# Optimization experiments

Measured on AMD Instinct MI355X. Metric: run time of the kernel, lower is better.

## Reference

```python
import jax, jax.numpy as jnp
import numpy as np

B, N, E, H, D, FF, L = 64, 200, 128, 8, 16, 512, 6
S = N + 1  # depot + nodes
EPS = 1e-5


def setup_inputs() -> dict:
    key = jax.random.key(0)
    ks = jax.random.split(key, 24)
    r = jax.random.normal
    HD = H * D
    inp = {
        "depot_xy": jax.random.uniform(ks[0], (B, 1, 3), dtype=jnp.float32),
        "node_xy_demand_tw": jax.random.uniform(ks[1], (B, N, 4), dtype=jnp.float32),
        "route_attn": r(ks[2], (B, H, S, S), dtype=jnp.float32),
        # initial embeddings
        "Wd": r(ks[3], (3, E)) * 0.3, "bd": jnp.zeros((E,)),
        "Wn": r(ks[4], (4, E)) * 0.3, "bn": jnp.zeros((E,)),
        # per-layer stacked params (leading dim L)
        "Wq": r(ks[5], (L, E, HD)) / np.sqrt(E),
        "Wk": r(ks[6], (L, E, HD)) / np.sqrt(E),
        "Wv": r(ks[7], (L, E, HD)) / np.sqrt(E),
        "Wo": r(ks[8], (L, HD, E)) / np.sqrt(HD), "bo": jnp.zeros((L, E)),
        # score_aggr MLP: in=head_num*aspect_num=2H, hidden=2H, out=H
        "A1w": r(ks[9], (L, 2 * H, 2 * H)) / np.sqrt(2 * H), "A1b": jnp.zeros((L, 2 * H)),
        "A2w": r(ks[10], (L, 2 * H, H)) / np.sqrt(2 * H), "A2b": jnp.zeros((L, H)),
        # instance-norm affine params
        "n1w": jnp.ones((L, E)), "n1b": jnp.zeros((L, E)),
        "n2w": jnp.ones((L, E)), "n2b": jnp.zeros((L, E)),
        # feed-forward
        "F1w": r(ks[11], (L, E, FF)) / np.sqrt(E), "F1b": jnp.zeros((L, FF)),
        "F2w": r(ks[12], (L, FF, E)) / np.sqrt(FF), "F2b": jnp.zeros((L, E)),
    }
    return inp


def _inorm(y, w, b):
    # InstanceNorm1d over the sequence axis (per batch, per channel), biased var, eps=1e-5
    m = jnp.mean(y, axis=1, keepdims=True)
    v = jnp.var(y, axis=1, keepdims=True)
    return (y - m) / jnp.sqrt(v + EPS) * w + b


def _encoder(depot_xy, node_xy_demand_tw, route_attn, Wd, bd, Wn, bn,
             Wq, Wk, Wv, Wo, bo, A1w, A1b, A2w, A2b,
             n1w, n1b, n2w, n2b, F1w, F1b, F2w, F2b):
    x = jnp.concatenate([depot_xy @ Wd + bd, node_xy_demand_tw @ Wn + bn], axis=1)  # [B,S,E]
    b, s = x.shape[0], x.shape[1]
    for l in range(L):
        heads = lambda t: t.reshape(b, s, H, D).transpose(0, 2, 1, 3)  # [B,H,S,D]
        q, k, v = heads(x @ Wq[l]), heads(x @ Wk[l]), heads(x @ Wv[l])
        score = jnp.einsum('bhnd,bhmd->bhnm', q, k)                    # [B,H,S,S]
        cat = jnp.concatenate([score, route_attn], axis=1)             # [B,2H,S,S]
        cat = cat.transpose(0, 2, 3, 1)                                # [B,S,S,2H]
        agg = jax.nn.relu(cat @ A1w[l] + A1b[l]) @ A2w[l] + A2b[l]     # [B,S,S,H]
        scaled = agg.transpose(0, 3, 1, 2)                             # [B,H,S,S]
        w = jax.nn.softmax(scaled, axis=-1)
        o = jnp.einsum('bhnm,bhmd->bhnd', w, v)                        # [B,H,S,D]
        o = o.transpose(0, 2, 1, 3).reshape(b, s, H * D)
        mh = o @ Wo[l] + bo[l]
        out1 = _inorm(x + mh, n1w[l], n1b[l])
        ff = jax.nn.relu(out1 @ F1w[l] + F1b[l]) @ F2w[l] + F2b[l]
        x = _inorm(out1 + ff, n2w[l], n2b[l])
    return x


def reference(depot_xy, node_xy_demand_tw, route_attn, Wd, bd, Wn, bn,
              Wq, Wk, Wv, Wo, bo, A1w, A1b, A2w, A2b,
              n1w, n1b, n2w, n2b, F1w, F1b, F2w, F2b):
    return _encoder(depot_xy, node_xy_demand_tw, route_attn, Wd, bd, Wn, bn,
                    Wq, Wk, Wv, Wo, bo, A1w, A1b, A2w, A2b,
                    n1w, n1b, n2w, n2b, F1w, F1b, F2w, F2b)
```

## Files before the change

kernel.cpp:

```cpp
#include <hip/hip_runtime.h>
#include <hip/hip_bf16.h>

#define B_   64
#define N_   200
#define S_   201
#define E_   128
#define H_   8
#define D_   16
#define HD_  128
#define FF_  512
#define L_   6
#define TWOH_ 16
#define NCH_  4
#define NCHB_ 51
#define PADM_ 209

typedef __hip_bfloat16 bf16;
typedef __attribute__((ext_vector_type(8))) short bfrag;
typedef __attribute__((ext_vector_type(4))) float f32x4;

__device__ __forceinline__ void split_bf16(float v, bf16& h, bf16& l) {
  h = __float2bfloat16(v);
  l = __float2bfloat16(v - __bfloat162float(h));
}

__global__ void embed_kernel(const float* __restrict__ depot, const float* __restrict__ node,
                             const float* __restrict__ Wd, const float* __restrict__ bd,
                             const float* __restrict__ Wn, const float* __restrict__ bn,
                             float* __restrict__ X, bf16* __restrict__ XBh, bf16* __restrict__ XBl) {
  int idx = blockIdx.x * blockDim.x + threadIdx.x;
  if (idx >= B_ * S_ * E_) return;
  int e  = idx & (E_ - 1);
  int bs = idx >> 7;
  int s  = bs % S_;
  int b  = bs / S_;
  float acc;
  if (s == 0) {
    acc = bd[e];
    #pragma unroll
    for (int i = 0; i < 3; ++i) acc += depot[b * 3 + i] * Wd[i * E_ + e];
  } else {
    acc = bn[e];
    const float* nd = node + ((size_t)b * N_ + (s - 1)) * 4;
    #pragma unroll
    for (int i = 0; i < 4; ++i) acc += nd[i] * Wn[i * E_ + e];
  }
  X[idx] = acc;
  bf16 hh, ll;
  split_bf16(acc, hh, ll);
  XBh[idx] = hh;
  XBl[idx] = ll;
}

__global__ void wcvt_kernel(const float* __restrict__ Wo, const float* __restrict__ F1w,
                            const float* __restrict__ F2w, const float* __restrict__ Wq,
                            const float* __restrict__ Wk, const float* __restrict__ Wv,
                            bf16* __restrict__ WTh, bf16* __restrict__ WTl) {
  int idx = blockIdx.x * blockDim.x + threadIdx.x;
  if (idx >= 1179648) return;
  float v;
  if (idx < 98304) {
    int l = idx / 16384, rr = idx % 16384;
    int e = rr / 128, h = rr % 128;
    v = Wo[(size_t)l * 16384 + h * 128 + e];
  } else if (idx < 491520) {
    int rem = idx - 98304;
    int l = rem / 65536, rr = rem % 65536;
    int f = rr / 128, e = rr % 128;
    v = F1w[(size_t)l * 65536 + e * 512 + f];
  } else if (idx < 884736) {
    int rem = idx - 491520;
    int l = rem / 65536, rr = rem % 65536;
    int e = rr / 512, f = rr % 512;
    v = F2w[(size_t)l * 65536 + f * 128 + e];
  } else if (idx < 1081344) {
    int rem = idx - 884736;
    int l = rem / 32768, rr = rem % 32768;
    int n = rr / 128, e = rr % 128;
    const float* src = (n < 128) ? Wq : Wk;
    int hd = n & 127;
    v = src[(size_t)l * 16384 + e * 128 + hd];
  } else {
    int rem = idx - 1081344;
    int l = rem / 16384, rr = rem % 16384;
    int hd = rr / 128, e = rr % 128;
    v = Wv[(size_t)l * 16384 + e * 128 + hd];
  }
  bf16 h, l2;
  split_bf16(v, h, l2);
  WTh[idx] = h;
  WTl[idx] = l2;
}

template<int EPI>
__global__ __launch_bounds__(256) void mgemm_kernel(
    const bf16* __restrict__ Ah, const bf16* __restrict__ Al,
    const bf16* __restrict__ BTh, const bf16* __restrict__ BTl,
    const float* __restrict__ bias, const float* __restrict__ res,
    float* __restrict__ Cf, bf16* __restrict__ Cbh, bf16* __restrict__ Cbl,
    int K, int Ntot) {
  __shared__ __align__(16) bf16 Ash[64][72];
  __shared__ __align__(16) bf16 Asl[64][72];
  __shared__ __align__(16) bf16 Bsh[64][72];
  __shared__ __align__(16) bf16 Bsl[64][72];
  int tid = threadIdx.x;
  int m0 = blockIdx.x * 64, n0 = blockIdx.y * 64;
  int lane = tid & 63, wave = tid >> 6;
  int wr = wave >> 1, wc = wave & 1;
  int la = lane & 15, lb = lane >> 4;
  f32x4 acc[2][2] = {};
  for (int k0 = 0; k0 < K; k0 += 64) {
    #pragma unroll
    for (int p = 0; p < 2; ++p) {
      int ch = tid + p * 256;
      int r = ch >> 3, kc = (ch & 7) << 3;
      size_t ga = (size_t)(m0 + r) * K + k0 + kc;
      size_t gb = (size_t)(n0 + r) * K + k0 + kc;
      *reinterpret_cast<bfrag*>(&Ash[r][kc]) = *reinterpret_cast<const bfrag*>(&Ah[ga]);
      *reinterpret_cast<bfrag*>(&Asl[r][kc]) = *reinterpret_cast<const bfrag*>(&Al[ga]);
      *reinterpret_cast<bfrag*>(&Bsh[r][kc]) = *reinterpret_cast<const bfrag*>(&BTh[gb]);
      *reinterpret_cast<bfrag*>(&Bsl[r][kc]) = *reinterpret_cast<const bfrag*>(&BTl[gb]);
    }
    __syncthreads();
    #pragma unroll
    for (int ks = 0; ks < 64; ks += 32) {
      bfrag ah0 = *(const bfrag*)&Ash[wr * 32 + la][ks + lb * 8];
      bfrag ah1 = *(const bfrag*)&Ash[wr * 32 + 16 + la][ks + lb * 8];
      bfrag al0 = *(const bfrag*)&Asl[wr * 32 + la][ks + lb * 8];
      bfrag al1 = *(const bfrag*)&Asl[wr * 32 + 16 + la][ks + lb * 8];
      bfrag bh0 = *(const bfrag*)&Bsh[wc * 32 + la][ks + lb * 8];
      bfrag bh1 = *(const bfrag*)&Bsh[wc * 32 + 16 + la][ks + lb * 8];
      bfrag bl0 = *(const bfrag*)&Bsl[wc * 32 + la][ks + lb * 8];
      bfrag bl1 = *(const bfrag*)&Bsl[wc * 32 + 16 + la][ks + lb * 8];
      acc[0][0] = __builtin_amdgcn_mfma_f32_16x16x32_bf16(ah0, bh0, acc[0][0], 0, 0, 0);
      acc[0][0] = __builtin_amdgcn_mfma_f32_16x16x32_bf16(ah0, bl0, acc[0][0], 0, 0, 0);
      acc[0][0] = __builtin_amdgcn_mfma_f32_16x16x32_bf16(al0, bh0, acc[0][0], 0, 0, 0);
      acc[0][1] = __builtin_amdgcn_mfma_f32_16x16x32_bf16(ah0, bh1, acc[0][1], 0, 0, 0);
      acc[0][1] = __builtin_amdgcn_mfma_f32_16x16x32_bf16(ah0, bl1, acc[0][1], 0, 0, 0);
      acc[0][1] = __builtin_amdgcn_mfma_f32_16x16x32_bf16(al0, bh1, acc[0][1], 0, 0, 0);
      acc[1][0] = __builtin_amdgcn_mfma_f32_16x16x32_bf16(ah1, bh0, acc[1][0], 0, 0, 0);
      acc[1][0] = __builtin_amdgcn_mfma_f32_16x16x32_bf16(ah1, bl0, acc[1][0], 0, 0, 0);
      acc[1][0] = __builtin_amdgcn_mfma_f32_16x16x32_bf16(al1, bh0, acc[1][0], 0, 0, 0);
      acc[1][1] = __builtin_amdgcn_mfma_f32_16x16x32_bf16(ah1, bh1, acc[1][1], 0, 0, 0);
      acc[1][1] = __builtin_amdgcn_mfma_f32_16x16x32_bf16(ah1, bl1, acc[1][1], 0, 0, 0);
      acc[1][1] = __builtin_amdgcn_mfma_f32_16x16x32_bf16(al1, bh1, acc[1][1], 0, 0, 0);
    }
    __syncthreads();
  }
  int r0 = lb * 4;
  #pragma unroll
  for (int ti = 0; ti < 2; ++ti)
    #pragma unroll
    for (int tj = 0; tj < 2; ++tj)
      #pragma unroll
      for (int j = 0; j < 4; ++j) {
        int m = m0 + wr * 32 + ti * 16 + r0 + j;
        int n = n0 + wc * 32 + tj * 16 + la;
        float v = acc[ti][tj][j];
        if (EPI == 1) {
          v += bias[n] + res[(size_t)m * Ntot + n];
          Cf[(size_t)m * Ntot + n] = v;
        } else if (EPI == 2) {
          v += bias[n];
          v = v > 0.f ? v : 0.f;
          bf16 vh, vl;
          split_bf16(v, vh, vl);
          Cbh[(size_t)m * Ntot + n] = vh;
          Cbl[(size_t)m * Ntot + n] = vl;
        } else {
          Cf[(size_t)m * Ntot + n] = v;
        }
      }
}

__global__ __launch_bounds__(256) void score_kernel(const float* __restrict__ QK,
                                                    float* __restrict__ SC) {
  int bh = blockIdx.x;
  int h = bh & 7, b = bh >> 3;
  int nbase = blockIdx.y * 51;
  int ncnt = min(51, S_ - nbase);
  __shared__ __align__(16) float qs[51][20];
  __shared__ __align__(16) float ks[S_][20];
  int tid = threadIdx.x;
  for (int p = tid; p < 51 * 16; p += 256) {
    int r = p >> 4, d = p & 15;
    if (r < ncnt) qs[r][d] = QK[((size_t)(b * S_ + nbase + r)) * 256 + h * D_ + d];
  }
  for (int p = tid; p < S_ * 16; p += 256) {
    int r = p >> 4, d = p & 15;
    ks[r][d] = QK[((size_t)(b * S_ + r)) * 256 + 128 + h * D_ + d];
  }
  __syncthreads();
  float* out = SC + ((size_t)(b * H_ + h)) * S_ * S_;
  int tn = tid >> 4, tm = tid & 15;
  for (int n0 = tn * 2; n0 < ncnt; n0 += 32) {
    int n1v = (n0 + 1 < ncnt);
    f32x4 q0[4], q1[4];
    #pragma unroll
    for (int qd = 0; qd < 4; ++qd) {
      q0[qd] = *(const f32x4*)&qs[n0][qd * 4];
      q1[qd] = *(const f32x4*)&qs[n1v ? n0 + 1 : n0][qd * 4];
    }
    for (int m0 = tm * 2; m0 < S_; m0 += 32) {
      int m1v = (m0 + 1 < S_);
      float a00 = 0, a01 = 0, a10 = 0, a11 = 0;
      #pragma unroll
      for (int qd = 0; qd < 4; ++qd) {
        f32x4 k0 = *(const f32x4*)&ks[m0][qd * 4];
        f32x4 k1 = *(const f32x4*)&ks[m1v ? m0 + 1 : m0][qd * 4];
        #pragma unroll
        for (int c = 0; c < 4; ++c) {
          a00 += q0[qd][c] * k0[c];
          a01 += q0[qd][c] * k1[c];
          a10 += q1[qd][c] * k0[c];
          a11 += q1[qd][c] * k1[c];
        }
      }
      int gn = nbase + n0;
      out[(size_t)gn * S_ + m0] = a00;
      if (m1v) out[(size_t)gn * S_ + m0 + 1] = a01;
      if (n1v) {
        out[(size_t)(gn + 1) * S_ + m0] = a10;
        if (m1v) out[(size_t)(gn + 1) * S_ + m0 + 1] = a11;
      }
    }
  }
}

__global__ __launch_bounds__(256) void attn_kernel(
    const float* __restrict__ SC, const float* __restrict__ RA,
    const float* __restrict__ A1w, const float* __restrict__ A1b,
    const float* __restrict__ A2w, const float* __restrict__ A2b,
    const float* __restrict__ V, bf16* __restrict__ OBh, bf16* __restrict__ OBl) {
  int blk = blockIdx.x;
  int b  = blk / NCHB_;
  int n0 = (blk % NCHB_) * NCH_;
  int NV = min(NCH_, S_ - n0);
  __shared__ float PL[NCH_][H_][PADM_];
  __shared__ float partial[2][NCH_][H_][D_];
  __shared__ float inv[NCH_][H_];
  int tid = threadIdx.x;

  {
    float cc[4][TWOH_];
    int   mm[4], nnv[4];
    bool  val[4];
    #pragma unroll
    for (int s = 0; s < 4; ++s) {
      int e = tid + s * 256;
      val[s] = (e < NV * S_);
      int nn = e / S_;
      int m  = e - nn * S_;
      if (!val[s]) { nn = 0; m = 0; }
      nnv[s] = nn; mm[s] = m;
      const float* scp = SC + (((size_t)b * H_) * S_ + (n0 + nn)) * S_ + m;
      const float* rap = RA + (((size_t)b * H_) * S_ + (n0 + nn)) * S_ + m;
      #pragma unroll
      for (int h = 0; h < H_; ++h) {
        cc[s][h]      = scp[(size_t)h * S_ * S_];
        cc[s][H_ + h] = rap[(size_t)h * S_ * S_];
      }
    }
    #pragma unroll
    for (int s = 0; s < 4; ++s) {
      if (!val[s]) continue;
      float h1[TWOH_];
      #pragma unroll
      for (int j = 0; j < TWOH_; ++j) h1[j] = A1b[j];
      #pragma unroll
      for (int i = 0; i < TWOH_; ++i) {
        float c = cc[s][i];
        #pragma unroll
        for (int j = 0; j < TWOH_; ++j)
          h1[j] += c * A1w[i * TWOH_ + j];
      }
      float agg[H_];
      #pragma unroll
      for (int h = 0; h < H_; ++h) agg[h] = A2b[h];
      #pragma unroll
      for (int j = 0; j < TWOH_; ++j) {
        float r = fmaxf(h1[j], 0.f);
        #pragma unroll
        for (int h = 0; h < H_; ++h)
          agg[h] += r * A2w[j * H_ + h];
      }
      #pragma unroll
      for (int h = 0; h < H_; ++h) PL[nnv[s]][h][mm[s]] = agg[h];
    }
  }
  __syncthreads();

  {
    int g = tid >> 3, lane = tid & 7;
    int nn = g >> 3, h = g & 7;
    if (nn < NV) {
      float mx = -1e30f;
      for (int m = lane; m < S_; m += 8) mx = fmaxf(mx, PL[nn][h][m]);
      #pragma unroll
      for (int off = 4; off > 0; off >>= 1) mx = fmaxf(mx, __shfl_xor(mx, off, 8));
      float sum = 0.f;
      for (int m = lane; m < S_; m += 8) {
        float e = __expf(PL[nn][h][m] - mx);
        PL[nn][h][m] = e;
        sum += e;
      }
      #pragma unroll
      for (int off = 4; off > 0; off >>= 1) sum += __shfl_xor(sum, off, 8);
      if (lane == 0) inv[nn][h] = 1.f / sum;
    }
  }
  __syncthreads();

  {
    int half = tid >> 7, h = (tid >> 4) & 7, d = tid & 15;
    float a0 = 0.f, a1 = 0.f, a2 = 0.f, a3 = 0.f;
    const float* vp = V + (size_t)b * S_ * HD_ + h * D_ + d;
    for (int m = half; m < S_; m += 2) {
      float vv = vp[(size_t)m * HD_];
      a0 += PL[0][h][m] * vv;
      a1 += PL[1][h][m] * vv;
      a2 += PL[2][h][m] * vv;
      a3 += PL[3][h][m] * vv;
    }
    partial[half][0][h][d] = a0;
    partial[half][1][h][d] = a1;
    partial[half][2][h][d] = a2;
    partial[half][3][h][d] = a3;
  }
  __syncthreads();
  if (tid < 128) {
    int h = tid >> 4, d = tid & 15;
    #pragma unroll
    for (int nn = 0; nn < NCH_; ++nn)
      if (nn < NV) {
        float s = (partial[0][nn][h][d] + partial[1][nn][h][d]) * inv[nn][h];
        size_t o = ((size_t)b * S_ + (n0 + nn)) * HD_ + h * D_ + d;
        bf16 sh, sl;
        split_bf16(s, sh, sl);
        OBh[o] = sh;
        OBl[o] = sl;
      }
  }
}

__global__ __launch_bounds__(512) void inorm_kernel(const float* __restrict__ Y,
                                                    const float* __restrict__ w,
                                                    const float* __restrict__ bb,
                                                    float* __restrict__ X,
                                                    bf16* __restrict__ XBh,
                                                    bf16* __restrict__ XBl) {
  int b = blockIdx.x;
  int tid = threadIdx.x;
  int e = tid & 127, sg = tid >> 7;
  __shared__ float ps[4][128], pss[4][128];
  const float* base = Y + (size_t)b * S_ * E_;
  float s = 0.f, ss = 0.f;
  for (int i = sg; i < S_; i += 4) {
    float v = base[(size_t)i * E_ + e];
    s += v; ss += v * v;
  }
  ps[sg][e] = s; pss[sg][e] = ss;
  __syncthreads();
  if (sg == 0) {
    s  = ps[0][e] + ps[1][e] + ps[2][e] + ps[3][e];
    ss = pss[0][e] + pss[1][e] + pss[2][e] + pss[3][e];
    float mean = s / S_;
    float var  = fmaxf(ss / S_ - mean * mean, 0.f);
    float scale = rsqrtf(var + 1e-5f) * w[e];
    ps[0][e]  = scale;
    pss[0][e] = bb[e] - mean * scale;
  }
  __syncthreads();
  float scale = ps[0][e], shift = pss[0][e];
  float* dst = X + (size_t)b * S_ * E_;
  for (int i = sg; i < S_; i += 4) {
    size_t idx = (size_t)i * E_ + e;
    float v = base[idx] * scale + shift;
    dst[idx] = v;
    if (XBh) {
      size_t gi = (size_t)b * S_ * E_ + idx;
      bf16 vh, vl;
      split_bf16(v, vh, vl);
      XBh[gi] = vh;
      XBl[gi] = vl;
    }
  }
}

extern "C" void kernel_launch(void* const* d_in, const int* in_sizes, int n_in,
                              void* d_out, int out_size, void* d_ws, size_t ws_size,
                              hipStream_t stream) {
  const float* depot = (const float*)d_in[0];
  const float* node  = (const float*)d_in[1];
  const float* RA    = (const float*)d_in[2];
  const float* Wd    = (const float*)d_in[3];
  const float* bd    = (const float*)d_in[4];
  const float* Wn    = (const float*)d_in[5];
  const float* bn    = (const float*)d_in[6];
  const float* Wq    = (const float*)d_in[7];
  const float* Wk    = (const float*)d_in[8];
  const float* Wv    = (const float*)d_in[9];
  const float* Wo    = (const float*)d_in[10];
  const float* bo    = (const float*)d_in[11];
  const float* A1w   = (const float*)d_in[12];
  const float* A1b   = (const float*)d_in[13];
  const float* A2w   = (const float*)d_in[14];
  const float* A2b   = (const float*)d_in[15];
  const float* n1w   = (const float*)d_in[16];
  const float* n1b   = (const float*)d_in[17];
  const float* n2w   = (const float*)d_in[18];
  const float* n2b   = (const float*)d_in[19];
  const float* F1w   = (const float*)d_in[20];
  const float* F1b   = (const float*)d_in[21];
  const float* F2w   = (const float*)d_in[22];
  const float* F2b   = (const float*)d_in[23];

  const size_t XSZ  = (size_t)B_ * S_ * E_;
  const size_t SCSZ = (size_t)B_ * H_ * S_ * S_;
  const size_t XBF  = XSZ / 2;
  float* ws = (float*)d_ws;
  float* X   = ws;
  float* QK  = ws + XSZ;
  float* V   = ws + 3 * XSZ;
  float* SC  = ws + 4 * XSZ;
  float* TMP = SC;
  bf16*  XBh = (bf16*)(SC + XSZ);
  bf16*  XBl = (bf16*)(SC + XSZ + XBF);
  bf16*  HBh = (bf16*)(SC + XSZ + 2 * XBF);
  bf16*  HBl = (bf16*)(SC + XSZ + 6 * XBF);
  float* tail = ws + 4 * XSZ + SCSZ;
  bf16*  WTh = (bf16*)tail;
  bf16*  WTl = (bf16*)(tail + 589824);
  bf16* OBh = (bf16*)QK;
  bf16* OBl = (bf16*)(ws + 2 * XSZ);

  const int M = B_ * S_;

  wcvt_kernel<<<4608, 256, 0, stream>>>(Wo, F1w, F2w, Wq, Wk, Wv, WTh, WTl);
  embed_kernel<<<(B_ * S_ * E_ + 255) / 256, 256, 0, stream>>>(depot, node, Wd, bd, Wn, bn, X, XBh, XBl);

  for (int l = 0; l < L_; ++l) {
    mgemm_kernel<3><<<dim3(M / 64, 4), 256, 0, stream>>>(
        XBh, XBl, WTh + 884736 + (size_t)l * 32768, WTl + 884736 + (size_t)l * 32768,
        nullptr, nullptr, QK, nullptr, nullptr, E_, 256);
    mgemm_kernel<3><<<dim3(M / 64, 2), 256, 0, stream>>>(
        XBh, XBl, WTh + 1081344 + (size_t)l * 16384, WTl + 1081344 + (size_t)l * 16384,
        nullptr, nullptr, V, nullptr, nullptr, E_, HD_);
    score_kernel<<<dim3(B_ * H_, 4), 256, 0, stream>>>(QK, SC);
    attn_kernel<<<B_ * NCHB_, 256, 0, stream>>>(SC, RA,
        A1w + (size_t)l * TWOH_ * TWOH_, A1b + (size_t)l * TWOH_,
        A2w + (size_t)l * TWOH_ * H_,    A2b + (size_t)l * H_, V, OBh, OBl);
    mgemm_kernel<1><<<dim3(M / 64, 2), 256, 0, stream>>>(
        OBh, OBl, WTh + (size_t)l * 16384, WTl + (size_t)l * 16384,
        bo + (size_t)l * E_, X, TMP, nullptr, nullptr, HD_, E_);
    inorm_kernel<<<B_, 512, 0, stream>>>(TMP, n1w + (size_t)l * E_, n1b + (size_t)l * E_, X, XBh, XBl);
    mgemm_kernel<2><<<dim3(M / 64, 8), 256, 0, stream>>>(
        XBh, XBl, WTh + 98304 + (size_t)l * 65536, WTl + 98304 + (size_t)l * 65536,
        F1b + (size_t)l * FF_, nullptr, nullptr, HBh, HBl, E_, FF_);
    mgemm_kernel<1><<<dim3(M / 64, 2), 256, 0, stream>>>(
        HBh, HBl, WTh + 491520 + (size_t)l * 65536, WTl + 491520 + (size_t)l * 65536,
        F2b + (size_t)l * E_, X, TMP, nullptr, nullptr, FF_, E_);
    float* dst = (l == L_ - 1) ? (float*)d_out : X;
    bf16* xh = (l == L_ - 1) ? nullptr : XBh;
    bf16* xl = (l == L_ - 1) ? nullptr : XBl;
    inorm_kernel<<<B_, 512, 0, stream>>>(TMP, n2w + (size_t)l * E_, n2b + (size_t)l * E_, dst, xh, xl);
  }
}
```

Measured before the change: 1.507 ms.

## Stage attention score rows in shared memory and split instance norm across channels

The attention kernel now handles 2 query rows per block instead of 4, doubling the block count. It first copies the score and route rows into shared memory with coalesced row-contiguous loads, then computes the per-element MLP from shared memory, replacing the strided per-head global gathers. The instance-norm kernel is split across 4 channel blocks per batch with 128 threads each, raising parallelism from 64 blocks to 256. The trade-offs are extra shared memory per block and less reuse of V loads in the attention kernel.

New measurement: 2.673 ms. +77.3%, slower.

```diff
diff --git a/kernel.cpp b/kernel.cpp
--- a/kernel.cpp
+++ b/kernel.cpp
@@ -11,9 +11,10 @@
 #define FF_  512
 #define L_   6
 #define TWOH_ 16
-#define NCH_  4
-#define NCHB_ 51
+#define NCH_  2
+#define NCHB_ 101
 #define PADM_ 209
+#define CATP_ 204
 
 typedef __hip_bfloat16 bf16;
 typedef __attribute__((ext_vector_type(8))) short bfrag;
@@ -236,76 +237,73 @@
   int b  = blk / NCHB_;
   int n0 = (blk % NCHB_) * NCH_;
   int NV = min(NCH_, S_ - n0);
+  __shared__ float cat[NCH_][TWOH_][CATP_];
   __shared__ float PL[NCH_][H_][PADM_];
   __shared__ float partial[2][NCH_][H_][D_];
   __shared__ float inv[NCH_][H_];
   int tid = threadIdx.x;
 
   {
-    float cc[4][TWOH_];
-    int   mm[4], nnv[4];
-    bool  val[4];
-    #pragma unroll
-    for (int s = 0; s < 4; ++s) {
-      int e = tid + s * 256;
-      val[s] = (e < NV * S_);
-      int nn = e / S_;
-      int m  = e - nn * S_;
-      if (!val[s]) { nn = 0; m = 0; }
-      nnv[s] = nn; mm[s] = m;
-      const float* scp = SC + (((size_t)b * H_) * S_ + (n0 + nn)) * S_ + m;
-      const float* rap = RA + (((size_t)b * H_) * S_ + (n0 + nn)) * S_ + m;
-      #pragma unroll
-      for (int h = 0; h < H_; ++h) {
-        cc[s][h]      = scp[(size_t)h * S_ * S_];
-        cc[s][H_ + h] = rap[(size_t)h * S_ * S_];
-      }
-    }
-    #pragma unroll
-    for (int s = 0; s < 4; ++s) {
-      if (!val[s]) continue;
-      float h1[TWOH_];
-      #pragma unroll
-      for (int j = 0; j < TWOH_; ++j) h1[j] = A1b[j];
-      #pragma unroll
-      for (int i = 0; i < TWOH_; ++i) {
-        float c = cc[s][i];
-        #pragma unroll
-        for (int j = 0; j < TWOH_; ++j)
-          h1[j] += c * A1w[i * TWOH_ + j];
-      }
-      float agg[H_];
-      #pragma unroll
-      for (int h = 0; h < H_; ++h) agg[h] = A2b[h];
-      #pragma unroll
-      for (int j = 0; j < TWOH_; ++j) {
-        float r = fmaxf(h1[j], 0.f);
-        #pragma unroll
-        for (int h = 0; h < H_; ++h)
-          agg[h] += r * A2w[j * H_ + h];
-      }
-      #pragma unroll
-      for (int h = 0; h < H_; ++h) PL[nnv[s]][h][mm[s]] = agg[h];
-    }
+    int total = NV * TWOH_ * S_;
+    for (int p = tid; p < total; p += 256) {
+      int r = p / S_;
+      int m = p - r * S_;
+      int nn = r >> 4, i = r & 15;
+      const float* src = (i < H_)
+        ? SC + (((size_t)b * H_ + i) * S_ + (n0 + nn)) * S_
+        : RA + (((size_t)b * H_ + (i - H_)) * S_ + (n0 + nn)) * S_;
+      cat[nn][i][m] = src[m];
+    }
+  }
+  __syncthreads();
+
+  for (int e = tid; e < NV * S_; e += 256) {
+    int nn = (e >= S_) ? 1 : 0;
+    int m  = e - nn * S_;
+    float cc[TWOH_];
+    #pragma unroll
+    for (int i = 0; i < TWOH_; ++i) cc[i] = cat[nn][i][m];
+    float h1[TWOH_];
+    #pragma unroll
+    for (int j = 0; j < TWOH_; ++j) h1[j] = A1b[j];
+    #pragma unroll
+    for (int i = 0; i < TWOH_; ++i) {
+      float c = cc[i];
+      #pragma unroll
+      for (int j = 0; j < TWOH_; ++j)
+        h1[j] += c * A1w[i * TWOH_ + j];
+    }
+    float agg[H_];
+    #pragma unroll
+    for (int h = 0; h < H_; ++h) agg[h] = A2b[h];
+    #pragma unroll
+    for (int j = 0; j < TWOH_; ++j) {
+      float r = fmaxf(h1[j], 0.f);
+      #pragma unroll
+      for (int h = 0; h < H_; ++h)
+        agg[h] += r * A2w[j * H_ + h];
+    }
+    #pragma unroll
+    for (int h = 0; h < H_; ++h) PL[nn][h][m] = agg[h];
   }
   __syncthreads();
 
   {
-    int g = tid >> 3, lane = tid & 7;
+    int g = tid >> 4, lane = tid & 15;
     int nn = g >> 3, h = g & 7;
     if (nn < NV) {
       float mx = -1e30f;
-      for (int m = lane; m < S_; m += 8) mx = fmaxf(mx, PL[nn][h][m]);
-      #pragma unroll
-      for (int off = 4; off > 0; off >>= 1) mx = fmaxf(mx, __shfl_xor(mx, off, 8));
+      for (int m = lane; m < S_; m += 16) mx = fmaxf(mx, PL[nn][h][m]);
+      #pragma unroll
+      for (int off = 8; off > 0; off >>= 1) mx = fmaxf(mx, __shfl_xor(mx, off, 16));
       float sum = 0.f;
-      for (int m = lane; m < S_; m += 8) {
+      for (int m = lane; m < S_; m += 16) {
         float e = __expf(PL[nn][h][m] - mx);
         PL[nn][h][m] = e;
         sum += e;
       }
       #pragma unroll
-      for (int off = 4; off > 0; off >>= 1) sum += __shfl_xor(sum, off, 8);
+      for (int off = 8; off > 0; off >>= 1) sum += __shfl_xor(sum, off, 16);
       if (lane == 0) inv[nn][h] = 1.f / sum;
     }
   }
@@ -313,19 +311,15 @@
 
   {
     int half = tid >> 7, h = (tid >> 4) & 7, d = tid & 15;
-    float a0 = 0.f, a1 = 0.f, a2 = 0.f, a3 = 0.f;
+    float a0 = 0.f, a1 = 0.f;
     const float* vp = V + (size_t)b * S_ * HD_ + h * D_ + d;
     for (int m = half; m < S_; m += 2) {
       float vv = vp[(size_t)m * HD_];
       a0 += PL[0][h][m] * vv;
       a1 += PL[1][h][m] * vv;
-      a2 += PL[2][h][m] * vv;
-      a3 += PL[3][h][m] * vv;
     }
     partial[half][0][h][d] = a0;
     partial[half][1][h][d] = a1;
-    partial[half][2][h][d] = a2;
-    partial[half][3][h][d] = a3;
   }
   __syncthreads();
   if (tid < 128) {
@@ -343,35 +337,37 @@
   }
 }
 
-__global__ __launch_bounds__(512) void inorm_kernel(const float* __restrict__ Y,
+__global__ __launch_bounds__(128) void inorm_kernel(const float* __restrict__ Y,
                                                     const float* __restrict__ w,
                                                     const float* __restrict__ bb,
                                                     float* __restrict__ X,
                                                     bf16* __restrict__ XBh,
                                                     bf16* __restrict__ XBl) {
   int b = blockIdx.x;
+  int e0 = blockIdx.y * 32;
   int tid = threadIdx.x;
-  int e = tid & 127, sg = tid >> 7;
-  __shared__ float ps[4][128], pss[4][128];
+  int el = tid & 31, sg = tid >> 5;
+  int e = e0 + el;
+  __shared__ float ps[4][32], pss[4][32];
   const float* base = Y + (size_t)b * S_ * E_;
   float s = 0.f, ss = 0.f;
   for (int i = sg; i < S_; i += 4) {
     float v = base[(size_t)i * E_ + e];
     s += v; ss += v * v;
   }
-  ps[sg][e] = s; pss[sg][e] = ss;
+  ps[sg][el] = s; pss[sg][el] = ss;
   __syncthreads();
   if (sg == 0) {
-    s  = ps[0][e] + ps[1][e] + ps[2][e] + ps[3][e];
-    ss = pss[0][e] + pss[1][e] + pss[2][e] + pss[3][e];
+    s  = ps[0][el] + ps[1][el] + ps[2][el] + ps[3][el];
+    ss = pss[0][el] + pss[1][el] + pss[2][el] + pss[3][el];
     float mean = s / S_;
     float var  = fmaxf(ss / S_ - mean * mean, 0.f);
     float scale = rsqrtf(var + 1e-5f) * w[e];
-    ps[0][e]  = scale;
-    pss[0][e] = bb[e] - mean * scale;
-  }
-  __syncthreads();
-  float scale = ps[0][e], shift = pss[0][e];
+    ps[0][el]  = scale;
+    pss[0][el] = bb[e] - mean * scale;
+  }
+  __syncthreads();
+  float scale = ps[0][el], shift = pss[0][el];
   float* dst = X + (size_t)b * S_ * E_;
   for (int i = sg; i < S_; i += 4) {
     size_t idx = (size_t)i * E_ + e;
@@ -453,7 +449,7 @@
     mgemm_kernel<1><<<dim3(M / 64, 2), 256, 0, stream>>>(
         OBh, OBl, WTh + (size_t)l * 16384, WTl + (size_t)l * 16384,
         bo + (size_t)l * E_, X, TMP, nullptr, nullptr, HD_, E_);
-    inorm_kernel<<<B_, 512, 0, stream>>>(TMP, n1w + (size_t)l * E_, n1b + (size_t)l * E_, X, XBh, XBl);
+    inorm_kernel<<<dim3(B_, 4), 128, 0, stream>>>(TMP, n1w + (size_t)l * E_, n1b + (size_t)l * E_, X, XBh, XBl);
     mgemm_kernel<2><<<dim3(M / 64, 8), 256, 0, stream>>>(
         XBh, XBl, WTh + 98304 + (size_t)l * 65536, WTl + 98304 + (size_t)l * 65536,
         F1b + (size_t)l * FF_, nullptr, nullptr, HBh, HBl, E_, FF_);
@@ -463,6 +459,6 @@
     float* dst = (l == L_ - 1) ? (float*)d_out : X;
     bf16* xh = (l == L_ - 1) ? nullptr : XBh;
     bf16* xl = (l == L_ - 1) ? nullptr : XBl;
-    inorm_kernel<<<B_, 512, 0, stream>>>(TMP, n2w + (size_t)l * E_, n2b + (size_t)l * E_, dst, xh, xl);
-  }
-}
+    inorm_kernel<<<dim3(B_, 4), 128, 0, stream>>>(TMP, n2w + (size_t)l * E_, n2b + (size_t)l * E_, dst, xh, xl);
+  }
+}
```
